# Kernel optimization log

Measured on AMD Instinct MI355X. Metric: run time of the kernel, lower is better.

Reference implementation:

```python
import jax, jax.numpy as jnp
import numpy as np

P_THRESH = 20  # p=0.2 * 100
# direction -> (di, dj): masked pixel (i,j) writes input[i,j] to x[i+di, j+dj], then avg to x[i,j]
OFFSETS = {0: (-1, -1), 1: (-1, 0), 2: (-1, 1), 3: (0, -1), 4: (0, 0), 5: (0, 1), 6: (1, -1), 7: (1, 0)}


def _shift(a, di, dj):
    """out[i+di, j+dj] = a[i, j] on last two axes; out-of-range -> 0/False."""
    H, W = a.shape[-2], a.shape[-1]
    pad = [(0, 0)] * (a.ndim - 2) + [(max(di, 0), max(-di, 0)), (max(dj, 0), max(-dj, 0))]
    p = jnp.pad(a, pad)
    sh, sw = max(-di, 0), max(-dj, 0)
    return p[..., sh:sh + H, sw:sw + W]


def _avg3x3_reflect(x):
    H, W = x.shape[-2], x.shape[-1]
    p = jnp.pad(x, [(0, 0), (0, 0), (1, 1), (1, 1)], mode='reflect')
    s = jnp.zeros_like(x)
    for i in range(3):
        for j in range(3):
            s = s + p[..., i:i + H, j:j + W]
    return s / 9.0


def brown_forward(input, dir, prob):
    avg = _avg3x3_reflect(input)
    pos = prob <= P_THRESH
    x = input
    for d in range(8):  # sequential, matching torch in-place write order
        di, dj = OFFSETS[d]
        m = (dir == d) & pos
        if d == 4:
            x = jnp.where(m, avg, x)  # mm: only avg write
        else:
            sm = _shift(m, di, dj)                       # neighbor-target mask
            x = jnp.where(sm, _shift(input, di, dj), x)  # x[i+di,j+dj] = input[i,j]
            mv = _shift(sm, -di, -dj)                    # mask restricted to valid region
            x = jnp.where(mv, avg, x)                    # x[i,j] = avg[i,j]
    return x


def setup_inputs() -> dict:
    key = jax.random.key(0)
    k1, k2, k3 = jax.random.split(key, 3)
    shape = (32, 64, 128, 128)
    return {
        'input': jax.random.normal(k1, shape, dtype=jnp.float32),
        'dir': jax.random.randint(k2, shape, 0, 8, dtype=jnp.int32),
        'prob': jax.random.randint(k3, shape, 1, 100, dtype=jnp.int32),
    }


def reference(input, dir, prob):
    return brown_forward(input, dir, prob)
```

## Files before the change

### kernel.cpp

```cpp
#include <hip/hip_runtime.h>
#include <cstddef>

#define H 128
#define W 128
#define TILE_R 32
#define P_THRESH 20

__global__ __launch_bounds__(256, 6)
void brown_kernel(const float* __restrict__ inp,
                  const int*  __restrict__ dirp,
                  const int*  __restrict__ prb,
                  float* __restrict__ out)
{
    const int tid   = threadIdx.x;
    const int bid   = blockIdx.x;
    const int slice = bid >> 2;
    const int r0    = (bid & 3) * TILE_R;
    const size_t base = (size_t)slice * (size_t)(H * W);

    const int cq  = tid & 31;
    const int rg  = tid >> 5;
    const int j0  = cq << 2;
    const int gi0 = r0 + (rg << 2);

    auto load_row = [&](int k, float v[6], unsigned& ma, unsigned& mb) {
        const int gr  = gi0 - 1 + k;
        const int gri = (gr < 0) ? 1 : ((gr >= H) ? (H - 2) : gr);
        const float4 c = ((const float4*)(inp + base + (size_t)gri * W))[cq];
        unsigned mwc;
        if ((unsigned)gr < (unsigned)H) {
            const int4 dv = ((const int4*)(dirp + base + (size_t)gr * W))[cq];
            const int4 pv = ((const int4*)(prb  + base + (size_t)gr * W))[cq];
            const unsigned a  = (pv.x <= P_THRESH) ? (unsigned)dv.x : 8u;
            const unsigned b  = (pv.y <= P_THRESH) ? (unsigned)dv.y : 8u;
            const unsigned cc = (pv.z <= P_THRESH) ? (unsigned)dv.z : 8u;
            const unsigned d  = (pv.w <= P_THRESH) ? (unsigned)dv.w : 8u;
            mwc = a | (b << 8) | (cc << 16) | (d << 24);
        } else {
            mwc = 0x08080808u;
        }
        const float    lf  = __shfl_up(c.w, 1);
        const float    rt  = __shfl_down(c.x, 1);
        const unsigned mwl = __shfl_up(mwc, 1);
        const unsigned mwr = __shfl_down(mwc, 1);
        v[1] = c.x; v[2] = c.y; v[3] = c.z; v[4] = c.w;
        v[0] = (cq > 0)  ? lf : c.y;
        v[5] = (cq < 31) ? rt : c.z;
        const unsigned ml = (cq > 0)  ? (mwl >> 24)  : 8u;
        const unsigned mr = (cq < 31) ? (mwr & 255u) : 8u;
        ma = (mwc << 8) | ml;
        mb = (mwc >> 8) | (mr << 24);
    };

    float va[6], vb[6], vc[6];
    unsigned maa, mab, mba, mbb, mca, mcb;
    load_row(0, va, maa, mab);
    load_row(1, vb, mba, mbb);

    #pragma unroll
    for (int rr = 0; rr < 4; ++rr) {
        load_row(rr + 2, vc, mca, mcb);

        const int gi = gi0 + rr;
        float cs[6];
        #pragma unroll
        for (int w = 0; w < 6; ++w) cs[w] = va[w] + vb[w] + vc[w];

        float4 res;
        float* rp = (float*)&res;
        #pragma unroll
        for (int p = 0; p < 4; ++p) {
            const float avg = (cs[p] + cs[p + 1] + cs[p + 2]) * (1.0f / 9.0f);
            const unsigned wTop = (p < 2) ? (maa >> (8 * p)) : (mab >> (8 * (p - 2)));
            const unsigned wMid = (p < 2) ? (mba >> (8 * p)) : (mbb >> (8 * (p - 2)));
            const unsigned wBot = (p < 2) ? (mca >> (8 * p)) : (mcb >> (8 * (p - 2)));

            float val = vb[p + 1];
            int dl = -1;
            if (((wBot >> 16) & 255u) == 0u) { val = vc[p + 2]; dl = 0; }
            if (((wBot >>  8) & 255u) == 1u) { val = vc[p + 1]; dl = 1; }
            if (( wBot        & 255u) == 2u) { val = vc[p];     dl = 2; }
            if (((wMid >> 16) & 255u) == 3u) { val = vb[p + 2]; dl = 3; }
            if (( wMid        & 255u) == 5u) { val = vb[p];     dl = 5; }
            if (((wTop >> 16) & 255u) == 6u) { val = va[p + 2]; dl = 6; }
            if (((wTop >>  8) & 255u) == 7u) { val = va[p + 1]; dl = 7; }

            const int msel = (int)((wMid >> 8) & 255u);
            const int q3 = (msel * 11) >> 5;
            const int di = q3 - 1;
            const int dj = msel - q3 * 3 - 1;
            const int ti = gi + di;
            const int tj = j0 + p + dj;
            const bool bok = (msel < 8) & ((unsigned)ti < 128u) & ((unsigned)tj < 128u);
            if (bok & (msel >= dl)) val = avg;
            rp[p] = val;
        }
        ((float4*)(out + base + (size_t)gi * W))[cq] = res;

        #pragma unroll
        for (int w = 0; w < 6; ++w) { va[w] = vb[w]; vb[w] = vc[w]; }
        maa = mba; mab = mbb; mba = mca; mbb = mcb;
    }
}

extern "C" void kernel_launch(void* const* d_in, const int* in_sizes, int n_in,
                              void* d_out, int out_size, void* d_ws, size_t ws_size,
                              hipStream_t stream) {
    const float* inp  = (const float*)d_in[0];
    const int*   dirp = (const int*)d_in[1];
    const int*   prb  = (const int*)d_in[2];
    float* out = (float*)d_out;

    const int slices = in_sizes[0] / (H * W);
    const int grid = slices * (H / TILE_R);
    brown_kernel<<<grid, 256, 0, stream>>>(inp, dirp, prb, out);
}
```

Measured before the change: 405.6 us.

## Restructure into per-slice blocks with double-buffered async global-to-LDS loads

Each block now handles a whole 128x128 slice with two waves. Each wave streams 8-row strips through double-buffered LDS using global_load_lds for the input, and prefetches dir/prob into registers one round ahead with manual vmcnt waits. Boundary validity checks are folded into the packed mask bytes at pack time, halo rows are shared across a strip instead of reloaded per 4-row group, and stores become nontemporal. The manual waitcnt accounting and cross-lane shuffles of masks add fragility, and the grid shrinks to one block per slice, which lowers parallelism.

```diff
diff --git a/kernel.cpp b/kernel.cpp
--- a/kernel.cpp
+++ b/kernel.cpp
@@ -3,103 +3,181 @@
 
 #define H 128
 #define W 128
-#define TILE_R 32
 #define P_THRESH 20
 
-__global__ __launch_bounds__(256, 6)
+typedef float nf2 __attribute__((ext_vector_type(2)));
+typedef __attribute__((address_space(1))) const unsigned int glo_u32;
+typedef __attribute__((address_space(3))) unsigned int lds_u32;
+
+__global__ __launch_bounds__(128, 4)
 void brown_kernel(const float* __restrict__ inp,
                   const int*  __restrict__ dirp,
                   const int*  __restrict__ prb,
                   float* __restrict__ out)
 {
-    const int tid   = threadIdx.x;
-    const int bid   = blockIdx.x;
-    const int slice = bid >> 2;
-    const int r0    = (bid & 3) * TILE_R;
-    const size_t base = (size_t)slice * (size_t)(H * W);
+    __shared__ __align__(16) float s_in[2 * 2 * 10 * W];
 
-    const int cq  = tid & 31;
-    const int rg  = tid >> 5;
-    const int j0  = cq << 2;
-    const int gi0 = r0 + (rg << 2);
+    const int tid  = threadIdx.x;
+    const int wid  = tid >> 6;
+    const int lane = tid & 63;
+    const size_t base = (size_t)blockIdx.x * (size_t)(H * W);
 
-    auto load_row = [&](int k, float v[6], unsigned& ma, unsigned& mb) {
-        const int gr  = gi0 - 1 + k;
-        const int gri = (gr < 0) ? 1 : ((gr >= H) ? (H - 2) : gr);
-        const float4 c = ((const float4*)(inp + base + (size_t)gri * W))[cq];
-        unsigned mwc;
-        if ((unsigned)gr < (unsigned)H) {
-            const int4 dv = ((const int4*)(dirp + base + (size_t)gr * W))[cq];
-            const int4 pv = ((const int4*)(prb  + base + (size_t)gr * W))[cq];
-            const unsigned a  = (pv.x <= P_THRESH) ? (unsigned)dv.x : 8u;
-            const unsigned b  = (pv.y <= P_THRESH) ? (unsigned)dv.y : 8u;
-            const unsigned cc = (pv.z <= P_THRESH) ? (unsigned)dv.z : 8u;
-            const unsigned d  = (pv.w <= P_THRESH) ? (unsigned)dv.w : 8u;
-            mwc = a | (b << 8) | (cc << 16) | (d << 24);
-        } else {
-            mwc = 0x08080808u;
+    float* sb0 = s_in + (wid * 2 + 0) * (10 * W);
+    float* sb1 = s_in + (wid * 2 + 1) * (10 * W);
+
+    const int hl  = lane >> 5;
+    const int cg  = lane & 31;
+    const int cgc = lane >> 1;
+    const int cgn = (lane & 1) ? ((cgc < 31) ? cgc + 1 : 31)
+                               : ((cgc > 0) ? cgc - 1 : 0);
+
+    int4 dv[5], pv[5];
+
+    auto issue_mk = [&](int wr0) {
+        #pragma unroll
+        for (int k = 0; k < 5; ++k) {
+            const int gr = wr0 - 1 + 2 * k + hl;
+            if ((unsigned)gr < (unsigned)H) {
+                dv[k] = ((const int4*)(dirp + base + (size_t)gr * W))[cg];
+                pv[k] = ((const int4*)(prb  + base + (size_t)gr * W))[cg];
+            } else {
+                dv[k] = make_int4(8, 8, 8, 8);
+                pv[k] = make_int4(100, 100, 100, 100);
+            }
         }
-        const float    lf  = __shfl_up(c.w, 1);
-        const float    rt  = __shfl_down(c.x, 1);
-        const unsigned mwl = __shfl_up(mwc, 1);
-        const unsigned mwr = __shfl_down(mwc, 1);
-        v[1] = c.x; v[2] = c.y; v[3] = c.z; v[4] = c.w;
-        v[0] = (cq > 0)  ? lf : c.y;
-        v[5] = (cq < 31) ? rt : c.z;
-        const unsigned ml = (cq > 0)  ? (mwl >> 24)  : 8u;
-        const unsigned mr = (cq < 31) ? (mwr & 255u) : 8u;
-        ma = (mwc << 8) | ml;
-        mb = (mwc >> 8) | (mr << 24);
+    };
+    auto issue_gl = [&](int wr0, float* sb) {
+        #pragma unroll
+        for (int k = 0; k < 5; ++k) {
+            const int idx = k * 64 + lane;
+            const int L   = idx >> 5;
+            const int c4  = idx & 31;
+            const int gr  = wr0 - 1 + L;
+            const int gri = (gr < 0) ? 1 : ((gr >= H) ? (H - 2) : gr);
+            const float* gp = inp + base + (size_t)gri * W + c4 * 4;
+            __builtin_amdgcn_global_load_lds((glo_u32*)gp, (lds_u32*)(sb + idx * 4), 16, 0, 0);
+        }
+        asm volatile("" ::: "memory");
+    };
+    auto pack = [&](int wr0, unsigned pk[5]) {
+        #pragma unroll
+        for (int k = 0; k < 5; ++k) {
+            const unsigned a = (pv[k].x <= P_THRESH) ? (unsigned)dv[k].x : 8u;
+            const unsigned b = (pv[k].y <= P_THRESH) ? (unsigned)dv[k].y : 8u;
+            const unsigned c = (pv[k].z <= P_THRESH) ? (unsigned)dv[k].z : 8u;
+            const unsigned d = (pv[k].w <= P_THRESH) ? (unsigned)dv[k].w : 8u;
+            unsigned m = a | (b << 8) | (c << 16) | (d << 24);
+            const int gr = wr0 - 1 + 2 * k + hl;
+            if (gr == 0) {
+                unsigned mm = 0;
+                #pragma unroll
+                for (int i2 = 0; i2 < 4; ++i2) {
+                    unsigned bb = (m >> (8 * i2)) & 255u;
+                    bb = (bb <= 2u) ? 8u : bb;
+                    mm |= bb << (8 * i2);
+                }
+                m = mm;
+            } else if (gr == H - 1) {
+                unsigned mm = 0;
+                #pragma unroll
+                for (int i2 = 0; i2 < 4; ++i2) {
+                    unsigned bb = (m >> (8 * i2)) & 255u;
+                    bb = (bb >= 6u) ? 8u : bb;
+                    mm |= bb << (8 * i2);
+                }
+                m = mm;
+            }
+            if (cg == 0) {
+                const unsigned b0 = m & 255u;
+                if ((0x49u >> b0) & 1u) m = (m & ~255u) | 8u;
+            }
+            if (cg == 31) {
+                const unsigned b3 = m >> 24;
+                if ((0x24u >> b3) & 1u) m = (m & 0x00FFFFFFu) | (8u << 24);
+            }
+            pk[k] = m;
+        }
     };
 
-    float va[6], vb[6], vc[6];
-    unsigned maa, mab, mba, mbb, mca, mcb;
-    load_row(0, va, maa, mab);
-    load_row(1, vb, mba, mbb);
+    auto round_compute = [&](int wr0, const float* sb, const unsigned pk[5]) {
+        unsigned maRow[10];
+        #pragma unroll
+        for (int L = 0; L < 10; ++L) {
+            const int sb5 = (L & 1) << 5;
+            const unsigned mwc = __shfl(pk[L >> 1], sb5 | cgc, 64);
+            const unsigned nw  = __shfl(pk[L >> 1], sb5 | cgn, 64);
+            const unsigned nb  = (lane == 0 || lane == 63) ? 8u
+                               : ((lane & 1) ? (nw & 255u) : (nw >> 24));
+            maRow[L] = (lane & 1) ? ((mwc >> 8) | (nb << 24))
+                                  : ((mwc << 8) | nb);
+        }
+        float va[4], vb_[4], vc_[4];
+        auto load_irow = [&](int L, float v[4]) {
+            const nf2 c = *((const nf2*)(sb + L * W) + lane);
+            const float lf = __shfl_up(c.y, 1);
+            const float rt = __shfl_down(c.x, 1);
+            v[1] = c.x; v[2] = c.y;
+            v[0] = (lane == 0)  ? c.y : lf;
+            v[3] = (lane == 63) ? c.x : rt;
+        };
+        load_irow(0, va);
+        load_irow(1, vb_);
+        #pragma unroll
+        for (int rr = 0; rr < 8; ++rr) {
+            load_irow(rr + 2, vc_);
+            const int gi = wr0 + rr;
+            float cs[4];
+            #pragma unroll
+            for (int w = 0; w < 4; ++w) cs[w] = va[w] + vb_[w] + vc_[w];
+            const unsigned maT = maRow[rr], maM = maRow[rr + 1], maB = maRow[rr + 2];
+            nf2 res;
+            #pragma unroll
+            for (int p = 0; p < 2; ++p) {
+                const float avg = (cs[p] + cs[p + 1] + cs[p + 2]) * (1.0f / 9.0f);
+                const unsigned wT = maT >> (8 * p);
+                const unsigned wM = maM >> (8 * p);
+                const unsigned wB = maB >> (8 * p);
+                float val = vb_[p + 1];
+                int dl = -1;
+                if (((wB >> 16) & 255u) == 0u) { val = vc_[p + 2]; dl = 0; }
+                if (((wB >>  8) & 255u) == 1u) { val = vc_[p + 1]; dl = 1; }
+                if (( wB        & 255u) == 2u) { val = vc_[p];     dl = 2; }
+                if (((wM >> 16) & 255u) == 3u) { val = vb_[p + 2]; dl = 3; }
+                if (( wM        & 255u) == 5u) { val = vb_[p];     dl = 5; }
+                if (((wT >> 16) & 255u) == 6u) { val = va[p + 2];  dl = 6; }
+                if (((wT >>  8) & 255u) == 7u) { val = va[p + 1];  dl = 7; }
+                const int msel = (int)((wM >> 8) & 255u);
+                if ((msel < 8) & (msel >= dl)) val = avg;
+                res[p] = val;
+            }
+            __builtin_nontemporal_store(res, (nf2*)(out + base + (size_t)gi * W) + lane);
+            #pragma unroll
+            for (int w = 0; w < 4; ++w) { va[w] = vb_[w]; vb_[w] = vc_[w]; }
+        }
+    };
 
-    #pragma unroll
-    for (int rr = 0; rr < 4; ++rr) {
-        load_row(rr + 2, vc, mca, mcb);
-
-        const int gi = gi0 + rr;
-        float cs[6];
-        #pragma unroll
-        for (int w = 0; w < 6; ++w) cs[w] = va[w] + vb[w] + vc[w];
-
-        float4 res;
-        float* rp = (float*)&res;
-        #pragma unroll
-        for (int p = 0; p < 4; ++p) {
-            const float avg = (cs[p] + cs[p + 1] + cs[p + 2]) * (1.0f / 9.0f);
-            const unsigned wTop = (p < 2) ? (maa >> (8 * p)) : (mab >> (8 * (p - 2)));
-            const unsigned wMid = (p < 2) ? (mba >> (8 * p)) : (mbb >> (8 * (p - 2)));
-            const unsigned wBot = (p < 2) ? (mca >> (8 * p)) : (mcb >> (8 * (p - 2)));
-
-            float val = vb[p + 1];
-            int dl = -1;
-            if (((wBot >> 16) & 255u) == 0u) { val = vc[p + 2]; dl = 0; }
-            if (((wBot >>  8) & 255u) == 1u) { val = vc[p + 1]; dl = 1; }
-            if (( wBot        & 255u) == 2u) { val = vc[p];     dl = 2; }
-            if (((wMid >> 16) & 255u) == 3u) { val = vb[p + 2]; dl = 3; }
-            if (( wMid        & 255u) == 5u) { val = vb[p];     dl = 5; }
-            if (((wTop >> 16) & 255u) == 6u) { val = va[p + 2]; dl = 6; }
-            if (((wTop >>  8) & 255u) == 7u) { val = va[p + 1]; dl = 7; }
-
-            const int msel = (int)((wMid >> 8) & 255u);
-            const int q3 = (msel * 11) >> 5;
-            const int di = q3 - 1;
-            const int dj = msel - q3 * 3 - 1;
-            const int ti = gi + di;
-            const int tj = j0 + p + dj;
-            const bool bok = (msel < 8) & ((unsigned)ti < 128u) & ((unsigned)tj < 128u);
-            if (bok & (msel >= dl)) val = avg;
-            rp[p] = val;
-        }
-        ((float4*)(out + base + (size_t)gi * W))[cq] = res;
-
-        #pragma unroll
-        for (int w = 0; w < 6; ++w) { va[w] = vb[w]; vb[w] = vc[w]; }
-        maa = mba; mab = mbb; mba = mca; mbb = mcb;
+    issue_gl(wid * 8, sb0);
+    issue_mk(wid * 8);
+    float* scur = sb0;
+    float* snxt = sb1;
+    for (int r = 0; r < 7; ++r) {
+        const int wr0 = r * 16 + wid * 8;
+        issue_gl(wr0 + 16, snxt);
+        unsigned pk[5];
+        pack(wr0, pk);
+        asm volatile("s_waitcnt vmcnt(13)" ::: "memory");
+        __builtin_amdgcn_sched_barrier(0);
+        issue_mk(wr0 + 16);
+        __builtin_amdgcn_sched_barrier(0);
+        round_compute(wr0, scur, pk);
+        float* t = scur; scur = snxt; snxt = t;
+    }
+    {
+        const int wr0 = 7 * 16 + wid * 8;
+        unsigned pk[5];
+        pack(wr0, pk);
+        asm volatile("s_waitcnt vmcnt(8)" ::: "memory");
+        round_compute(wr0, scur, pk);
     }
 }
 
@@ -112,6 +190,5 @@
     float* out = (float*)d_out;
 
     const int slices = in_sizes[0] / (H * W);
-    const int grid = slices * (H / TILE_R);
-    brown_kernel<<<grid, 256, 0, stream>>>(inp, dirp, prb, out);
+    brown_kernel<<<slices, 128, 0, stream>>>(inp, dirp, prb, out);
 }
```

Result: slower. 414.0 us (+2.1%).
